# Performance work log

Measured on AMD Instinct MI355X. Metric: run time of the kernel, lower is better.

Reference implementation:

```python
import jax, jax.numpy as jnp
import numpy as np

N, B, T, H, M, DM, K = 256, 32, 128, 64, 8, 32, 3
IN_DIM = 1
OUT_DIM = 1
DEC_H = H + DM  # 96


def _p(key, shape):
    return jax.random.normal(key, shape, jnp.float32) / np.sqrt(shape[0]).astype(np.float32)


def setup_inputs() -> dict:
    key = jax.random.key(0)
    ks = jax.random.split(key, 10)
    gdi = 2 * K * (IN_DIM + H)      # 390
    ddi = 2 * K * (OUT_DIM + DEC_H)  # 582
    return {
        'x': jax.random.normal(ks[0], (B, T, N, IN_DIM), jnp.float32),
        'Memory': _p(ks[1], (M, DM)),
        'Wq': _p(ks[2], (H, DM)),
        'We1': _p(ks[3], (N, M)),
        'We2': _p(ks[4], (N, M)),
        'enc_gate_w': _p(ks[5], (gdi, 2 * H)), 'enc_gate_b': jnp.zeros((2 * H,), jnp.float32),
        'enc_upd_w': _p(ks[6], (gdi, H)), 'enc_upd_b': jnp.zeros((H,), jnp.float32),
        'dec_gate_w': _p(ks[7], (ddi, 2 * DEC_H)), 'dec_gate_b': jnp.zeros((2 * DEC_H,), jnp.float32),
        'dec_upd_w': _p(ks[8], (ddi, DEC_H)), 'dec_upd_b': jnp.zeros((DEC_H,), jnp.float32),
        'proj_w': _p(ks[9], (DEC_H, OUT_DIM)), 'proj_b': jnp.zeros((OUT_DIM,), jnp.float32),
    }


def _cheb(s):
    # Chebyshev polynomials T_0..T_{K-1} of support s: [I, s, 2 s T_{k-1} - T_{k-2}]
    polys = [jnp.eye(N, dtype=s.dtype), s]
    for _ in range(2, K):
        polys.append(2.0 * s @ polys[-1] - polys[-2])
    return polys


def _scaled_lap(e1, e2, gkey):
    # cosine-similarity graph -> straight-through gumbel hard selection -> scaled Laplacian
    norm = jnp.linalg.norm(e1, axis=1, keepdims=True) @ jnp.linalg.norm(e2, axis=1, keepdims=True).T
    g = (e1 @ e2.T) / (norm + 1e-6)
    g = (g + 1.0) / 2.0
    logits = jnp.stack([g, 1.0 - g], axis=-1)               # (N,N,2)
    y_soft = logits + jax.random.gumbel(gkey, logits.shape, logits.dtype)  # tau=1 (note: source skips softmax)
    y_hard = jax.nn.one_hot(jnp.argmax(y_soft, axis=-1), 2, dtype=logits.dtype)
    adj = (y_hard - jax.lax.stop_gradient(y_soft) + y_soft)[:, :, 0]
    eye = jnp.eye(N, dtype=adj.dtype)
    adj = adj * (1.0 - eye)                                  # zero diagonal
    d = jnp.sum(adj, axis=1)
    L = jnp.diag(d) - adj
    lam = L.max() - L.min()
    return 2.0 * L / lam - eye


def _gconv(x, S, w, b):
    # S: (2K,N,N) stacked cheb supports; x: (B,N,C)
    xg = jnp.einsum('knm,bmc->bnkc', S, x)
    xg = xg.reshape(xg.shape[0], xg.shape[1], -1)            # (B,N,2K*C), support-major like torch cat
    return xg @ w + b


def _cell(x, state, S, gw, gb, uw, ub, hid):
    zr = jax.nn.sigmoid(_gconv(jnp.concatenate([x, state], -1), S, gw, gb))
    z, r = zr[..., :hid], zr[..., hid:]
    hc = jnp.tanh(_gconv(jnp.concatenate([x, z * state], -1), S, uw, ub))
    return r * state + (1.0 - r) * hc


def reference(x, Memory, Wq, We1, We2, enc_gate_w, enc_gate_b, enc_upd_w, enc_upd_b,
              dec_gate_w, dec_gate_b, dec_upd_w, dec_upd_b, proj_w, proj_b):
    k1, k2 = jax.random.split(jax.random.key(42))
    e1, e2 = We1 @ Memory, We2 @ Memory
    S = jnp.stack(_cheb(_scaled_lap(e1, e2, k1)) + _cheb(_scaled_lap(e2, e1, k2)))  # (2K,N,N)

    # --- encoder (1 layer) over time ---
    def enc_step(state, xt):
        h = _cell(xt, state, S, enc_gate_w, enc_gate_b, enc_upd_w, enc_upd_b, H)
        return h, None
    h0 = jnp.zeros((x.shape[0], N, H), x.dtype)
    h_t, _ = jax.lax.scan(enc_step, h0, jnp.swapaxes(x, 0, 1))

    # --- memory attention query ---
    query = h_t @ Wq                                        # (B,N,DM)
    att = jax.nn.softmax(query @ Memory.T, axis=-1)         # (B,N,M)
    value = att @ Memory                                    # (B,N,DM)
    h_de = jnp.concatenate([h_t, value], -1)                # (B,N,DEC_H)

    go0 = jnp.zeros((x.shape[0], N, OUT_DIM), x.dtype)
    def dec_step(carry, _):
        state, go = carry
        h = _cell(go, state, S, dec_gate_w, dec_gate_b, dec_upd_w, dec_upd_b, DEC_H)
        go = h @ proj_w + proj_b
        return (h, go), go
    _, outs = jax.lax.scan(dec_step, (h_de, go0), None, length=T)
    return jnp.swapaxes(outs, 0, 1)                         # (B,T,N,OUT_DIM)
```

## Files before the change

kernel.cpp:

```cpp
#include <hip/hip_runtime.h>
#include <stdint.h>
#include <math.h>

#define NNODE 256
#define BATCH 32
#define TLEN  128
#define ROWS  8192

typedef unsigned short u16;
typedef short bf16x8 __attribute__((ext_vector_type(8)));
typedef float f32x4 __attribute__((ext_vector_type(4)));

__device__ inline u16 f2bf_rn(float v) {
  uint32_t u = __float_as_uint(v);
  u += 0x7fffu + ((u >> 16) & 1u);
  return (u16)(u >> 16);
}
__device__ inline float bf2f(u16 h) { return __uint_as_float(((uint32_t)h) << 16); }
__device__ inline void split2(float v, u16& hi, u16& lo) {
  hi = f2bf_rn(v);
  lo = f2bf_rn(v - bf2f(hi));
}

__device__ inline size_t pk_addr(int c, int b, int n) {
  return ((((size_t)(c >> 4) * 32 + b) * 8 + (n >> 5)) << 9) +
         (((size_t)((c & 15) | (((n >> 3) & 3) << 4))) << 3) + (n & 7);
}

__host__ __device__ inline uint32_t rotl32_(uint32_t v, int d) {
  return (v << d) | (v >> (32 - d));
}
__host__ __device__ inline void tf2x32(uint32_t k0, uint32_t k1, uint32_t x0,
                                       uint32_t x1, uint32_t* o0, uint32_t* o1) {
  uint32_t ks2 = k0 ^ k1 ^ 0x1BD11BDAu;
  x0 += k0; x1 += k1;
  x0 += x1; x1 = rotl32_(x1, 13); x1 ^= x0;
  x0 += x1; x1 = rotl32_(x1, 15); x1 ^= x0;
  x0 += x1; x1 = rotl32_(x1, 26); x1 ^= x0;
  x0 += x1; x1 = rotl32_(x1, 6);  x1 ^= x0;
  x0 += k1; x1 += ks2 + 1u;
  x0 += x1; x1 = rotl32_(x1, 17); x1 ^= x0;
  x0 += x1; x1 = rotl32_(x1, 29); x1 ^= x0;
  x0 += x1; x1 = rotl32_(x1, 16); x1 ^= x0;
  x0 += x1; x1 = rotl32_(x1, 24); x1 ^= x0;
  x0 += ks2; x1 += k0 + 2u;
  x0 += x1; x1 = rotl32_(x1, 13); x1 ^= x0;
  x0 += x1; x1 = rotl32_(x1, 15); x1 ^= x0;
  x0 += x1; x1 = rotl32_(x1, 26); x1 ^= x0;
  x0 += x1; x1 = rotl32_(x1, 6);  x1 ^= x0;
  x0 += k0; x1 += k1 + 3u;
  x0 += x1; x1 = rotl32_(x1, 17); x1 ^= x0;
  x0 += x1; x1 = rotl32_(x1, 29); x1 ^= x0;
  x0 += x1; x1 = rotl32_(x1, 16); x1 ^= x0;
  x0 += x1; x1 = rotl32_(x1, 24); x1 ^= x0;
  x0 += k1; x1 += ks2 + 4u;
  x0 += x1; x1 = rotl32_(x1, 13); x1 ^= x0;
  x0 += x1; x1 = rotl32_(x1, 15); x1 ^= x0;
  x0 += x1; x1 = rotl32_(x1, 26); x1 ^= x0;
  x0 += x1; x1 = rotl32_(x1, 6);  x1 ^= x0;
  x0 += ks2; x1 += k0 + 5u;
  *o0 = x0; *o1 = x1;
}

__device__ inline float gumbel_at(uint32_t k0, uint32_t k1, uint32_t idx) {
  uint32_t o0, o1;
  tf2x32(k0, k1, 0u, idx, &o0, &o1);
  uint32_t b = o0 ^ o1;
  float f = __uint_as_float((b >> 9) | 0x3f800000u) - 1.0f;
  const float tiny = 1.17549435e-38f;
  float u = fmaxf(tiny, f + tiny);
  return -logf(-logf(u));
}

__global__ __launch_bounds__(256) void setup_embed_kernel(
    const float* __restrict__ We1, const float* __restrict__ We2,
    const float* __restrict__ Mem, float* __restrict__ e1, float* __restrict__ e2,
    float* __restrict__ n1, float* __restrict__ n2) {
  int n = threadIdx.x;
  float a[8];
  float s;
  for (int m = 0; m < 8; ++m) a[m] = We1[n * 8 + m];
  s = 0.f;
  for (int j = 0; j < 32; ++j) {
    float v = 0.f;
    for (int m = 0; m < 8; ++m) v = fmaf(a[m], Mem[m * 32 + j], v);
    e1[n * 32 + j] = v;
    s = fmaf(v, v, s);
  }
  n1[n] = sqrtf(s);
  for (int m = 0; m < 8; ++m) a[m] = We2[n * 8 + m];
  s = 0.f;
  for (int j = 0; j < 32; ++j) {
    float v = 0.f;
    for (int m = 0; m < 8; ++m) v = fmaf(a[m], Mem[m * 32 + j], v);
    e2[n * 32 + j] = v;
    s = fmaf(v, v, s);
  }
  n2[n] = sqrtf(s);
}

__global__ void stats_init_kernel(int* stats) {
  stats[0] = 0;
  stats[1] = 0;
  stats[2] = 0x7fffffff;
}

__global__ __launch_bounds__(256) void adj_kernel(
    const float* __restrict__ eA, const float* __restrict__ eB,
    const float* __restrict__ nA, const float* __restrict__ nB,
    uint32_t k0, uint32_t k1, float* __restrict__ adj, float* __restrict__ deg,
    int* __restrict__ stats) {
  int i = blockIdx.x, j = threadIdx.x;
  float dot = 0.f;
  for (int c = 0; c < 32; ++c) dot = fmaf(eA[i * 32 + c], eB[j * 32 + c], dot);
  float g = dot / (nA[i] * nB[j] + 1e-6f);
  g = (g + 1.0f) * 0.5f;
  uint32_t f = ((uint32_t)(i * 256 + j)) * 2u;
  float g0 = gumbel_at(k0, k1, f);
  float g1 = gumbel_at(k0, k1, f + 1u);
  float a = ((g + g0) >= ((1.0f - g) + g1)) ? 1.0f : 0.0f;
  if (i == j) a = 0.0f;
  adj[i * 256 + j] = a;
  __shared__ float red[256];
  red[j] = a;
  __syncthreads();
  for (int s = 128; s > 0; s >>= 1) {
    if (j < s) red[j] += red[j + s];
    __syncthreads();
  }
  if (j == 0) {
    float d = red[0];
    deg[i] = d;
    atomicMax(&stats[0], (int)d);
    atomicMin(&stats[2], (int)d);
    if (d > 0.5f) atomicOr(&stats[1], 1);
  }
}

__global__ __launch_bounds__(256) void lap_kernel(const float* __restrict__ adj,
                                                  const float* __restrict__ deg,
                                                  const int* __restrict__ stats,
                                                  float* __restrict__ S1) {
  int i = blockIdx.x, j = threadIdx.x;
  float lmax = (float)stats[0];
  float lmin = stats[1] ? -1.0f : (float)stats[2];
  float lam = lmax - lmin;
  float L = (i == j) ? deg[i] : -adj[i * 256 + j];
  S1[i * 256 + j] = 2.0f * L / lam - ((i == j) ? 1.0f : 0.0f);
}

__global__ __launch_bounds__(256) void t2_kernel(const float* __restrict__ A,
                                                 float* __restrict__ Cout) {
  __shared__ __align__(16) float sAT[32][68];
  __shared__ __align__(16) float sB[32][68];
  int tid = threadIdx.x;
  int tc = tid & 15, tr = tid >> 4;
  int row0 = blockIdx.y * 64, col0 = blockIdx.x * 64;
  float acc[4][4] = {};
  for (int m0 = 0; m0 < 256; m0 += 32) {
    for (int i = tid; i < 2048; i += 256) {
      int r = i >> 5, c = i & 31;
      sAT[c][r] = A[(size_t)(row0 + r) * 256 + m0 + c];
    }
    for (int i = tid; i < 2048; i += 256) {
      int r = i >> 6, c = i & 63;
      sB[r][c] = A[(size_t)(m0 + r) * 256 + col0 + c];
    }
    __syncthreads();
#pragma unroll
    for (int kk = 0; kk < 32; ++kk) {
      float4 av = *(const float4*)&sAT[kk][tr * 4];
      float4 bv = *(const float4*)&sB[kk][tc * 4];
      float a[4] = {av.x, av.y, av.z, av.w};
      float b[4] = {bv.x, bv.y, bv.z, bv.w};
#pragma unroll
      for (int i = 0; i < 4; ++i)
#pragma unroll
        for (int j = 0; j < 4; ++j) acc[i][j] = fmaf(a[i], b[j], acc[i][j]);
    }
    __syncthreads();
  }
#pragma unroll
  for (int i = 0; i < 4; ++i) {
    int row = row0 + tr * 4 + i;
#pragma unroll
    for (int j = 0; j < 4; ++j) {
      int col = col0 + tc * 4 + j;
      Cout[(size_t)row * 256 + col] = 2.0f * acc[i][j] - ((row == col) ? 1.0f : 0.0f);
    }
  }
}

__global__ void cvt_s_packed(const float* __restrict__ S, u16* __restrict__ Sh,
                             u16* __restrict__ Sl) {
  int idx = blockIdx.x * 256 + threadIdx.x;
  if (idx >= 4 * 65536) return;
  int p = idx >> 16, rem = idx & 65535;
  int n = rem >> 8, m = rem & 255;
  int nt = n >> 4, li = n & 15;
  int mc = m >> 5, g = (m >> 3) & 3, j = m & 7;
  int lane = li | (g << 4);
  size_t a = (((size_t)(p * 16 + nt) * 8 + mc) << 9) + lane * 8 + j;
  u16 h, l;
  split2(S[idx], h, l);
  Sh[a] = h; Sl[a] = l;
}

__global__ void build_wfrag(const float* __restrict__ W, int C, int O, int hid,
                            u16* __restrict__ WfH, u16* __restrict__ WfL,
                            float* __restrict__ w0, float* __restrict__ wlast) {
  int idx = blockIdx.x * 256 + threadIdx.x;
  int nKC = hid / 32;
  if (idx < 5 * hid * O) {
    int kk = idx & 31;
    int rest = idx >> 5;
    int o = rest % O; rest /= O;
    int kc = rest % nKC;
    int p = rest / nKC;
    int korig = (p == 0) ? 0 : (p + (p >= 3 ? 1 : 0));
    int c = kc * 32 + kk;
    float v = 0.f;
    if (c > 0) {
      v = W[(size_t)(korig * C + c) * O + o];
      if (p == 0) v += W[(size_t)(3 * C + c) * O + o];
    }
    int ot = o >> 4, li = o & 15, g = kk >> 3, j = kk & 7;
    int lane = li | (g << 4);
    size_t a = (((size_t)(p * nKC + kc) * (O / 16) + ot) << 9) + lane * 8 + j;
    u16 h, l; split2(v, h, l);
    WfH[a] = h; WfL[a] = l;
  }
  if (idx < 5 * O) {
    int o = idx % O, p = idx / O;
    int korig = (p == 0) ? 0 : (p + (p >= 3 ? 1 : 0));
    float v0 = W[(size_t)(korig * C + 0) * O + o];
    if (p == 0) v0 += W[(size_t)(3 * C + 0) * O + o];
    w0[p * O + o] = v0;
    float vl = W[(size_t)(korig * C + hid) * O + o];
    if (p == 0) vl += W[(size_t)(3 * C + hid) * O + o];
    wlast[p * O + o] = vl;
  }
}

__global__ void zero_kernel(uint4* __restrict__ p, int n4) {
  for (int i = blockIdx.x * blockDim.x + threadIdx.x; i < n4;
       i += gridDim.x * blockDim.x)
    p[i] = make_uint4(0, 0, 0, 0);
}

__global__ void enc_init(const float* __restrict__ x, float* __restrict__ hf,
                         u16* __restrict__ pkh, u16* __restrict__ pkl) {
  int idx = blockIdx.x * 256 + threadIdx.x;
  if (idx >= 65 * ROWS) return;
  int c = idx / ROWS, col = idx % ROWS;
  int b = col >> 8, n = col & 255;
  float v = (c == 0) ? x[(size_t)b * (TLEN * NNODE) + n] : 0.f;
  hf[idx] = v;
  if (c == 0) {
    u16 h, l; split2(v, h, l);
    size_t a = pk_addr(0, b, n);
    pkh[a] = h; pkl[a] = l;
  }
}

__global__ __launch_bounds__(128) void attn2(const float* __restrict__ hEf,
                                             const float* __restrict__ Wq,
                                             const float* __restrict__ Mem,
                                             float* __restrict__ hDf,
                                             u16* __restrict__ pkh,
                                             u16* __restrict__ pkl) {
  int col = blockIdx.x * 128 + threadIdx.x;
  int b = col >> 8, n = col & 255;
  float h[64];
  for (int c = 0; c < 64; ++c) h[c] = hEf[(size_t)(1 + c) * ROWS + col];
  float q[32];
  for (int j = 0; j < 32; ++j) {
    float s = 0.f;
    for (int c = 0; c < 64; ++c) s = fmaf(h[c], Wq[c * 32 + j], s);
    q[j] = s;
  }
  float l[8], mx = -3.402823466e38f;
  for (int m = 0; m < 8; ++m) {
    float s = 0.f;
    for (int j = 0; j < 32; ++j) s = fmaf(q[j], Mem[m * 32 + j], s);
    l[m] = s;
    mx = fmaxf(mx, s);
  }
  float se = 0.f;
  for (int m = 0; m < 8; ++m) { l[m] = expf(l[m] - mx); se += l[m]; }
  float val[32];
  for (int j = 0; j < 32; ++j) {
    float v = 0.f;
    for (int m = 0; m < 8; ++m) v = fmaf(l[m] / se, Mem[m * 32 + j], v);
    val[j] = v;
  }
  for (int c = 0; c < 97; ++c) {
    float v = (c == 0) ? 0.f : ((c <= 64) ? h[c - 1] : val[c - 65]);
    hDf[(size_t)c * ROWS + col] = v;
    u16 hh, ll; split2(v, hh, ll);
    size_t a = pk_addr(c, b, n);
    pkh[a] = hh; pkl[a] = ll;
  }
}

template <int C, int HID, int CPAD, int O, int NKC, int MT1, int MODE>
__global__ __launch_bounds__(1024, 4) void fused_step(
    const float* __restrict__ AF,
    const u16* __restrict__ ApkH, const u16* __restrict__ ApkL,
    const u16* __restrict__ SpkH, const u16* __restrict__ SpkL,
    const u16* __restrict__ WpkH, const u16* __restrict__ WpkL,
    const float* __restrict__ w0, const float* __restrict__ wlast,
    const float* __restrict__ bias,
    float* __restrict__ HF, float* __restrict__ outF,
    u16* __restrict__ outPkH, u16* __restrict__ outPkL,
    float* __restrict__ rbuf,
    const float* __restrict__ xsrc, int tnext,
    const float* __restrict__ pw, const float* __restrict__ pb,
    float* __restrict__ outp, int tcur) {
  constexpr int MT2 = O / 16;
  constexpr int MT1A = (MT1 + 1) / 2;
  constexpr int CH0SLOT = HID + 1;

  __shared__ __align__(16) u16 Gh[2][5][16][CPAD];
  __shared__ __align__(16) u16 Gl[2][5][16][CPAD];
  __shared__ float projL[(MODE == 2) ? 2 : 1][16][(MODE == 2) ? 100 : 1];

  const int tid = threadIdx.x;
  const int wid = tid >> 6, lane = tid & 63;
  const int g = lane >> 4, li = lane & 15;
  const int cg = wid >> 3, pp = wid & 3, half = (wid >> 2) & 1;
  const int bid0 = (int)blockIdx.x;
  const int bidx = ((bid0 & 7) << 5) | (bid0 >> 3);
  const int col0 = bidx * 32;
  const int b = col0 >> 8;
  const int n0 = (col0 & 255) + cg * 16;
  const int nt = n0 >> 4;

  for (int i = tid; i < 32 * C; i += 1024) {
    int c = i >> 5, q = i & 31;
    float v = AF[(size_t)c * ROWS + col0 + q];
    u16 h, l; split2(v, h, l);
    int slot = (c == 0) ? CH0SLOT : c;
    Gh[q >> 4][0][q & 15][slot] = h;
    Gl[q >> 4][0][q & 15][slot] = l;
  }
  if (tid < 32) {
    Gh[tid >> 4][0][tid & 15][0] = 0;
    Gl[tid >> 4][0][tid & 15][0] = 0;
  }

  f32x4 acc1[MT1A];
#pragma unroll
  for (int i = 0; i < MT1A; ++i) acc1[i] = (f32x4){0.f, 0.f, 0.f, 0.f};

#pragma unroll 2
  for (int mc = 0; mc < 8; ++mc) {
    size_t sa = (((size_t)(pp * 16 + nt) * 8 + mc) << 9) + lane * 8;
    bf16x8 sbh = *(const bf16x8*)(SpkH + sa);
    bf16x8 sbl = *(const bf16x8*)(SpkL + sa);
#pragma unroll
    for (int i = 0; i < MT1A; ++i) {
      const int mt = half * MT1A + i;
      if (mt < MT1) {
        size_t aa = (((size_t)(mt * 32 + b) * 8 + mc) << 9) + lane * 8;
        bf16x8 ah = *(const bf16x8*)(ApkH + aa);
        bf16x8 al = *(const bf16x8*)(ApkL + aa);
        acc1[i] = __builtin_amdgcn_mfma_f32_16x16x32_bf16(ah, sbh, acc1[i], 0, 0, 0);
        acc1[i] = __builtin_amdgcn_mfma_f32_16x16x32_bf16(ah, sbl, acc1[i], 0, 0, 0);
        acc1[i] = __builtin_amdgcn_mfma_f32_16x16x32_bf16(al, sbh, acc1[i], 0, 0, 0);
      }
    }
  }

  {
    const int p = pp + 1;
#pragma unroll
    for (int i = 0; i < MT1A; ++i) {
      const int mt = half * MT1A + i;
      if (mt < MT1) {
        int cq = mt * 16 + 4 * g;
        u16 h4[4], l4[4];
#pragma unroll
        for (int r = 0; r < 4; ++r) split2(acc1[i][r], h4[r], l4[r]);
        if (cq == 0) {
          Gh[cg][p][li][CH0SLOT] = h4[0];
          Gl[cg][p][li][CH0SLOT] = l4[0];
          h4[0] = 0; l4[0] = 0;
        }
        if (cq + 3 <= HID) {
          uint2 vh, vl;
          vh.x = (uint32_t)h4[0] | ((uint32_t)h4[1] << 16);
          vh.y = (uint32_t)h4[2] | ((uint32_t)h4[3] << 16);
          vl.x = (uint32_t)l4[0] | ((uint32_t)l4[1] << 16);
          vl.y = (uint32_t)l4[2] | ((uint32_t)l4[3] << 16);
          *(uint2*)&Gh[cg][p][li][cq] = vh;
          *(uint2*)&Gl[cg][p][li][cq] = vl;
        } else {
#pragma unroll
          for (int r = 0; r < 4; ++r) {
            int c = cq + r;
            if (c >= 1 && c <= HID) {
              Gh[cg][p][li][c] = h4[r];
              Gl[cg][p][li][c] = l4[r];
            }
          }
        }
      }
    }
  }
  __syncthreads();

  const int mt2 = wid;
  f32x4 acc2[2];
  acc2[0] = (f32x4){0.f, 0.f, 0.f, 0.f};
  acc2[1] = (f32x4){0.f, 0.f, 0.f, 0.f};
  if (mt2 < MT2) {
#pragma unroll
    for (int p = 0; p < 5; ++p) {
#pragma unroll
      for (int kc = 0; kc < NKC; ++kc) {
        bf16x8 bh[2], bl[2];
#pragma unroll
        for (int c2 = 0; c2 < 2; ++c2) {
          bh[c2] = *(const bf16x8*)&Gh[c2][p][li][kc * 32 + g * 8];
          bl[c2] = *(const bf16x8*)&Gl[c2][p][li][kc * 32 + g * 8];
        }
        size_t wa = (((size_t)(p * NKC + kc) * MT2 + mt2) << 9) + lane * 8;
        bf16x8 wh = *(const bf16x8*)(WpkH + wa);
        bf16x8 wl = *(const bf16x8*)(WpkL + wa);
#pragma unroll
        for (int c2 = 0; c2 < 2; ++c2) {
          acc2[c2] = __builtin_amdgcn_mfma_f32_16x16x32_bf16(wh, bh[c2], acc2[c2], 0, 0, 0);
          acc2[c2] = __builtin_amdgcn_mfma_f32_16x16x32_bf16(wh, bl[c2], acc2[c2], 0, 0, 0);
          acc2[c2] = __builtin_amdgcn_mfma_f32_16x16x32_bf16(wl, bh[c2], acc2[c2], 0, 0, 0);
        }
      }
    }
  }

  float ch0v[2][5], clv[2][5];
#pragma unroll
  for (int c2 = 0; c2 < 2; ++c2)
#pragma unroll
    for (int p = 0; p < 5; ++p) {
      ch0v[c2][p] = (p == 0)
          ? AF[col0 + c2 * 16 + li]
          : (bf2f(Gh[c2][p][li][CH0SLOT]) + bf2f(Gl[c2][p][li][CH0SLOT]));
      clv[c2][p] = bf2f(Gh[c2][p][li][HID]) + bf2f(Gl[c2][p][li][HID]);
    }

  if (mt2 < MT2) {
#pragma unroll
    for (int c2 = 0; c2 < 2; ++c2) {
      const int colx = col0 + c2 * 16 + li;
      const int ncolx = colx & 255;
#pragma unroll
      for (int r = 0; r < 4; ++r) {
        int o = mt2 * 16 + 4 * g + r;
        float v = acc2[c2][r] + bias[o];
#pragma unroll
        for (int p = 0; p < 5; ++p) {
          v = fmaf(w0[p * O + o], ch0v[c2][p], v);
          v = fmaf(wlast[p * O + o], clv[c2][p], v);
        }
        if (MODE == 0) {
          float s = 1.0f / (1.0f + expf(-v));
          if (o < HID) {
            float u = s * HF[(size_t)(1 + o) * ROWS + colx];
            outF[(size_t)(1 + o) * ROWS + colx] = u;
            u16 h_, l_; split2(u, h_, l_);
            size_t a = pk_addr(1 + o, b, ncolx);
            outPkH[a] = h_; outPkL[a] = l_;
          } else {
            rbuf[(size_t)(o - HID) * ROWS + colx] = s;
          }
        } else {
          float hc = tanhf(v);
          float hp = HF[(size_t)(1 + o) * ROWS + colx];
          float rr = rbuf[(size_t)o * ROWS + colx];
          float hn = rr * hp + (1.0f - rr) * hc;
          HF[(size_t)(1 + o) * ROWS + colx] = hn;
          u16 h_, l_; split2(hn, h_, l_);
          size_t a = pk_addr(1 + o, b, ncolx);
          outPkH[a] = h_; outPkL[a] = l_;
          if (MODE == 2) projL[c2][li][o] = hn;
        }
      }
    }
  }

  if (MODE == 0) {
    if (tid < 32) {
      int cc = col0 + tid;
      float x0 = AF[cc];
      outF[cc] = x0;
      u16 h_, l_; split2(x0, h_, l_);
      size_t a = pk_addr(0, b, cc & 255);
      outPkH[a] = h_; outPkL[a] = l_;
    }
  }
  if (MODE == 1) {
    __syncthreads();
    if (tid < 32) {
      int cc = col0 + tid;
      int n = cc & 255;
      float xv = (tnext >= 0)
          ? xsrc[(size_t)b * (TLEN * NNODE) + (size_t)tnext * NNODE + n]
          : HF[cc];
      HF[cc] = xv;
      u16 h_, l_; split2(xv, h_, l_);
      size_t a = pk_addr(0, b, n);
      outPkH[a] = h_; outPkL[a] = l_;
    }
  }
  if (MODE == 2) {
    __syncthreads();
    if (tid < 32) {
      int cc = col0 + tid;
      int n = cc & 255;
      float s = pb[0];
#pragma unroll
      for (int o = 0; o < HID; ++o) s = fmaf(pw[o], projL[tid >> 4][tid & 15][o], s);
      HF[cc] = s;
      u16 h_, l_; split2(s, h_, l_);
      size_t a = pk_addr(0, b, n);
      outPkH[a] = h_; outPkL[a] = l_;
      outp[((size_t)b * TLEN + tcur) * NNODE + n] = s;
    }
  }
}

extern "C" void kernel_launch(void* const* d_in, const int* in_sizes, int n_in,
                              void* d_out, int out_size, void* d_ws, size_t ws_size,
                              hipStream_t stream) {
  (void)in_sizes; (void)n_in; (void)out_size; (void)ws_size;
  const float* x   = (const float*)d_in[0];
  const float* Mem = (const float*)d_in[1];
  const float* Wq  = (const float*)d_in[2];
  const float* We1 = (const float*)d_in[3];
  const float* We2 = (const float*)d_in[4];
  const float* egw = (const float*)d_in[5];
  const float* egb = (const float*)d_in[6];
  const float* euw = (const float*)d_in[7];
  const float* eub = (const float*)d_in[8];
  const float* dgw = (const float*)d_in[9];
  const float* dgb = (const float*)d_in[10];
  const float* duw = (const float*)d_in[11];
  const float* dub = (const float*)d_in[12];
  const float* pw  = (const float*)d_in[13];
  const float* pb  = (const float*)d_in[14];
  float* out = (float*)d_out;

  float* ws = (float*)d_ws;
  size_t off = 0;
  auto allocf = [&](size_t nf) {
    float* p = ws + off;
    off += (nf + 63) & ~(size_t)63;
    return p;
  };
  auto allocu = [&](size_t nu) { return (u16*)allocf((nu + 1) / 2); };

  float* Sf  = allocf(4 * 65536);
  float* e1  = allocf(8192);
  float* e2  = allocf(8192);
  float* n1  = allocf(256);
  float* n2  = allocf(256);
  float* adj = allocf(65536);
  float* deg = allocf(256);
  int* stats = (int*)allocf(64);
  float* rb  = allocf((size_t)96 * ROWS);
  float* hEf = allocf((size_t)65 * ROWS);
  float* uEf = allocf((size_t)65 * ROWS);
  float* hDf = allocf((size_t)97 * ROWS);
  float* uDf = allocf((size_t)97 * ROWS);
  float* w0gE = allocf(5 * 128);
  float* w0uE = allocf(5 * 64);
  float* w0gD = allocf(5 * 192);
  float* w0uD = allocf(5 * 96);
  float* wlgE = allocf(5 * 128);
  float* wluE = allocf(5 * 64);
  float* wlgD = allocf(5 * 192);
  float* wluD = allocf(5 * 96);

  u16* SpkH = allocu((size_t)4 * 65536);
  u16* SpkL = allocu((size_t)4 * 65536);
  u16* WgEh = allocu((size_t)5 * 2 * 8 * 512);
  u16* WgEl = allocu((size_t)5 * 2 * 8 * 512);
  u16* WuEh = allocu((size_t)5 * 2 * 4 * 512);
  u16* WuEl = allocu((size_t)5 * 2 * 4 * 512);
  u16* WgDh = allocu((size_t)5 * 3 * 12 * 512);
  u16* WgDl = allocu((size_t)5 * 3 * 12 * 512);
  u16* WuDh = allocu((size_t)5 * 3 * 6 * 512);
  u16* WuDl = allocu((size_t)5 * 3 * 6 * 512);

  const size_t PKE = (size_t)5 * 32 * 8 * 512;
  const size_t PKD = (size_t)7 * 32 * 8 * 512;
  u16* hEpkH = allocu(PKE);
  u16* hEpkL = allocu(PKE);
  u16* uEpkH = allocu(PKE);
  u16* uEpkL = allocu(PKE);
  u16* hDpkH = allocu(PKD);
  u16* hDpkL = allocu(PKD);
  u16* uDpkH = allocu(PKD);
  u16* uDpkL = allocu(PKD);
  const size_t PKTOT = 4 * PKE + 4 * PKD;

  uint32_t ka0, ka1, kb0, kb1;
  tf2x32(0u, 42u, 0u, 0u, &ka0, &ka1);
  tf2x32(0u, 42u, 0u, 1u, &kb0, &kb1);

  zero_kernel<<<1024, 256, 0, stream>>>((uint4*)hEpkH, (int)(PKTOT / 8));
  setup_embed_kernel<<<1, 256, 0, stream>>>(We1, We2, Mem, e1, e2, n1, n2);
  stats_init_kernel<<<1, 1, 0, stream>>>(stats);
  adj_kernel<<<256, 256, 0, stream>>>(e1, e2, n1, n2, ka0, ka1, adj, deg, stats);
  lap_kernel<<<256, 256, 0, stream>>>(adj, deg, stats, Sf);
  t2_kernel<<<dim3(4, 4), 256, 0, stream>>>(Sf, Sf + 65536);
  stats_init_kernel<<<1, 1, 0, stream>>>(stats);
  adj_kernel<<<256, 256, 0, stream>>>(e2, e1, n2, n1, kb0, kb1, adj, deg, stats);
  lap_kernel<<<256, 256, 0, stream>>>(adj, deg, stats, Sf + 2 * 65536);
  t2_kernel<<<dim3(4, 4), 256, 0, stream>>>(Sf + 2 * 65536, Sf + 3 * 65536);
  cvt_s_packed<<<1024, 256, 0, stream>>>(Sf, SpkH, SpkL);
  build_wfrag<<<(5 * 64 * 128 + 255) / 256, 256, 0, stream>>>(egw, 65, 128, 64, WgEh, WgEl, w0gE, wlgE);
  build_wfrag<<<(5 * 64 * 64 + 255) / 256, 256, 0, stream>>>(euw, 65, 64, 64, WuEh, WuEl, w0uE, wluE);
  build_wfrag<<<(5 * 96 * 192 + 255) / 256, 256, 0, stream>>>(dgw, 97, 192, 96, WgDh, WgDl, w0gD, wlgD);
  build_wfrag<<<(5 * 96 * 96 + 255) / 256, 256, 0, stream>>>(duw, 97, 96, 96, WuDh, WuDl, w0uD, wluD);

  enc_init<<<(65 * ROWS + 255) / 256, 256, 0, stream>>>(x, hEf, hEpkH, hEpkL);
  for (int t = 0; t < TLEN; ++t) {
    fused_step<65, 64, 72, 128, 2, 5, 0><<<256, 1024, 0, stream>>>(
        hEf, hEpkH, hEpkL, SpkH, SpkL, WgEh, WgEl, w0gE, wlgE, egb,
        hEf, uEf, uEpkH, uEpkL, rb, nullptr, -1, nullptr, nullptr, nullptr, 0);
    fused_step<65, 64, 72, 64, 2, 5, 1><<<256, 1024, 0, stream>>>(
        uEf, uEpkH, uEpkL, SpkH, SpkL, WuEh, WuEl, w0uE, wluE, eub,
        hEf, hEf, hEpkH, hEpkL, rb,
        x, (t + 1 < TLEN) ? (t + 1) : -1, nullptr, nullptr, nullptr, 0);
  }

  attn2<<<64, 128, 0, stream>>>(hEf, Wq, Mem, hDf, hDpkH, hDpkL);

  for (int t = 0; t < TLEN; ++t) {
    fused_step<97, 96, 104, 192, 3, 7, 0><<<256, 1024, 0, stream>>>(
        hDf, hDpkH, hDpkL, SpkH, SpkL, WgDh, WgDl, w0gD, wlgD, dgb,
        hDf, uDf, uDpkH, uDpkL, rb, nullptr, -1, nullptr, nullptr, nullptr, 0);
    fused_step<97, 96, 104, 96, 3, 7, 2><<<256, 1024, 0, stream>>>(
        uDf, uDpkH, uDpkL, SpkH, SpkL, WuDh, WuDl, w0uD, wluD, dub,
        hDf, hDf, hDpkH, hDpkL, rb,
        nullptr, -1, pw, pb, out, t);
  }
}
```

Baseline: 8.907 ms.

## Drop fp32 state copies and keep recurrent state only in split-bf16 packed form

Removes the fp32 channel-major state buffers (hEf/uEf/hDf/uDf). Every stage now reads the previous hidden state and gate inputs by reconstructing hi+lo bf16 pairs from the packed buffers, so each step writes and reads less global memory and no longer re-splits fp32 data. The shared-memory G tiles move from padded [16][CPAD] rows to a blocked 8-element layout, which changes LDS bank access for the 16-byte fragment reads. The price is a small precision loss, since state passes through a two-term bf16 representation instead of full fp32. The packed-address reads in the prologue are also more scattered than the old contiguous fp32 rows.

```diff
diff --git a/kernel.cpp b/kernel.cpp
--- a/kernel.cpp
+++ b/kernel.cpp
@@ -248,31 +248,30 @@
     p[i] = make_uint4(0, 0, 0, 0);
 }
 
-__global__ void enc_init(const float* __restrict__ x, float* __restrict__ hf,
+__global__ void enc_init(const float* __restrict__ x,
                          u16* __restrict__ pkh, u16* __restrict__ pkl) {
-  int idx = blockIdx.x * 256 + threadIdx.x;
-  if (idx >= 65 * ROWS) return;
-  int c = idx / ROWS, col = idx % ROWS;
+  int col = blockIdx.x * 256 + threadIdx.x;
+  if (col >= ROWS) return;
   int b = col >> 8, n = col & 255;
-  float v = (c == 0) ? x[(size_t)b * (TLEN * NNODE) + n] : 0.f;
-  hf[idx] = v;
-  if (c == 0) {
-    u16 h, l; split2(v, h, l);
-    size_t a = pk_addr(0, b, n);
-    pkh[a] = h; pkl[a] = l;
-  }
-}
-
-__global__ __launch_bounds__(128) void attn2(const float* __restrict__ hEf,
+  float v = x[(size_t)b * (TLEN * NNODE) + n];
+  u16 h, l; split2(v, h, l);
+  size_t a = pk_addr(0, b, n);
+  pkh[a] = h; pkl[a] = l;
+}
+
+__global__ __launch_bounds__(128) void attn2(const u16* __restrict__ hEh,
+                                             const u16* __restrict__ hEl,
                                              const float* __restrict__ Wq,
                                              const float* __restrict__ Mem,
-                                             float* __restrict__ hDf,
                                              u16* __restrict__ pkh,
                                              u16* __restrict__ pkl) {
   int col = blockIdx.x * 128 + threadIdx.x;
   int b = col >> 8, n = col & 255;
   float h[64];
-  for (int c = 0; c < 64; ++c) h[c] = hEf[(size_t)(1 + c) * ROWS + col];
+  for (int c = 0; c < 64; ++c) {
+    size_t a = pk_addr(1 + c, b, n);
+    h[c] = bf2f(hEh[a]) + bf2f(hEl[a]);
+  }
   float q[32];
   for (int j = 0; j < 32; ++j) {
     float s = 0.f;
@@ -296,22 +295,20 @@
   }
   for (int c = 0; c < 97; ++c) {
     float v = (c == 0) ? 0.f : ((c <= 64) ? h[c - 1] : val[c - 65]);
-    hDf[(size_t)c * ROWS + col] = v;
     u16 hh, ll; split2(v, hh, ll);
     size_t a = pk_addr(c, b, n);
     pkh[a] = hh; pkl[a] = ll;
   }
 }
 
-template <int C, int HID, int CPAD, int O, int NKC, int MT1, int MODE>
+template <int C, int HID, int O, int NKC, int MT1, int MODE>
 __global__ __launch_bounds__(1024, 4) void fused_step(
-    const float* __restrict__ AF,
     const u16* __restrict__ ApkH, const u16* __restrict__ ApkL,
     const u16* __restrict__ SpkH, const u16* __restrict__ SpkL,
     const u16* __restrict__ WpkH, const u16* __restrict__ WpkL,
     const float* __restrict__ w0, const float* __restrict__ wlast,
     const float* __restrict__ bias,
-    float* __restrict__ HF, float* __restrict__ outF,
+    const u16* __restrict__ stH, const u16* __restrict__ stL,
     u16* __restrict__ outPkH, u16* __restrict__ outPkL,
     float* __restrict__ rbuf,
     const float* __restrict__ xsrc, int tnext,
@@ -320,33 +317,39 @@
   constexpr int MT2 = O / 16;
   constexpr int MT1A = (MT1 + 1) / 2;
   constexpr int CH0SLOT = HID + 1;
-
-  __shared__ __align__(16) u16 Gh[2][5][16][CPAD];
-  __shared__ __align__(16) u16 Gl[2][5][16][CPAD];
-  __shared__ float projL[(MODE == 2) ? 2 : 1][16][(MODE == 2) ? 100 : 1];
+  constexpr int KS8 = (HID + 9) / 8;
+
+  __shared__ __align__(16) u16 GhR[(size_t)2 * 5 * KS8 * 16 * 8];
+  __shared__ __align__(16) u16 GlR[(size_t)2 * 5 * KS8 * 16 * 8];
+  __shared__ float projL[(MODE == 2) ? 32 * 100 : 4];
+
+  auto Gidx = [](int c2, int p, int li, int slot) -> size_t {
+    return (((size_t)((c2 * 5 + p) * KS8 + (slot >> 3)) * 16 + li) << 3) +
+           (slot & 7);
+  };
 
   const int tid = threadIdx.x;
   const int wid = tid >> 6, lane = tid & 63;
   const int g = lane >> 4, li = lane & 15;
-  const int cg = wid >> 3, pp = wid & 3, half = (wid >> 2) & 1;
+  const int cgi = wid >> 3, pp = wid & 3, half = (wid >> 2) & 1;
   const int bid0 = (int)blockIdx.x;
   const int bidx = ((bid0 & 7) << 5) | (bid0 >> 3);
   const int col0 = bidx * 32;
   const int b = col0 >> 8;
-  const int n0 = (col0 & 255) + cg * 16;
+  const int nb = col0 & 255;
+  const int n0 = nb + cgi * 16;
   const int nt = n0 >> 4;
 
   for (int i = tid; i < 32 * C; i += 1024) {
     int c = i >> 5, q = i & 31;
-    float v = AF[(size_t)c * ROWS + col0 + q];
-    u16 h, l; split2(v, h, l);
+    size_t a = pk_addr(c, b, nb + q);
     int slot = (c == 0) ? CH0SLOT : c;
-    Gh[q >> 4][0][q & 15][slot] = h;
-    Gl[q >> 4][0][q & 15][slot] = l;
+    GhR[Gidx(q >> 4, 0, q & 15, slot)] = ApkH[a];
+    GlR[Gidx(q >> 4, 0, q & 15, slot)] = ApkL[a];
   }
   if (tid < 32) {
-    Gh[tid >> 4][0][tid & 15][0] = 0;
-    Gl[tid >> 4][0][tid & 15][0] = 0;
+    GhR[Gidx(tid >> 4, 0, tid & 15, 0)] = 0;
+    GlR[Gidx(tid >> 4, 0, tid & 15, 0)] = 0;
   }
 
   f32x4 acc1[MT1A];
@@ -383,8 +386,8 @@
 #pragma unroll
         for (int r = 0; r < 4; ++r) split2(acc1[i][r], h4[r], l4[r]);
         if (cq == 0) {
-          Gh[cg][p][li][CH0SLOT] = h4[0];
-          Gl[cg][p][li][CH0SLOT] = l4[0];
+          GhR[Gidx(cgi, p, li, CH0SLOT)] = h4[0];
+          GlR[Gidx(cgi, p, li, CH0SLOT)] = l4[0];
           h4[0] = 0; l4[0] = 0;
         }
         if (cq + 3 <= HID) {
@@ -393,15 +396,15 @@
           vh.y = (uint32_t)h4[2] | ((uint32_t)h4[3] << 16);
           vl.x = (uint32_t)l4[0] | ((uint32_t)l4[1] << 16);
           vl.y = (uint32_t)l4[2] | ((uint32_t)l4[3] << 16);
-          *(uint2*)&Gh[cg][p][li][cq] = vh;
-          *(uint2*)&Gl[cg][p][li][cq] = vl;
+          *(uint2*)&GhR[Gidx(cgi, p, li, cq)] = vh;
+          *(uint2*)&GlR[Gidx(cgi, p, li, cq)] = vl;
         } else {
 #pragma unroll
           for (int r = 0; r < 4; ++r) {
             int c = cq + r;
             if (c >= 1 && c <= HID) {
-              Gh[cg][p][li][c] = h4[r];
-              Gl[cg][p][li][c] = l4[r];
+              GhR[Gidx(cgi, p, li, c)] = h4[r];
+              GlR[Gidx(cgi, p, li, c)] = l4[r];
             }
           }
         }
@@ -422,8 +425,8 @@
         bf16x8 bh[2], bl[2];
 #pragma unroll
         for (int c2 = 0; c2 < 2; ++c2) {
-          bh[c2] = *(const bf16x8*)&Gh[c2][p][li][kc * 32 + g * 8];
-          bl[c2] = *(const bf16x8*)&Gl[c2][p][li][kc * 32 + g * 8];
+          bh[c2] = *(const bf16x8*)&GhR[Gidx(c2, p, li, kc * 32 + g * 8)];
+          bl[c2] = *(const bf16x8*)&GlR[Gidx(c2, p, li, kc * 32 + g * 8)];
         }
         size_t wa = (((size_t)(p * NKC + kc) * MT2 + mt2) << 9) + lane * 8;
         bf16x8 wh = *(const bf16x8*)(WpkH + wa);
@@ -443,17 +446,21 @@
   for (int c2 = 0; c2 < 2; ++c2)
 #pragma unroll
     for (int p = 0; p < 5; ++p) {
-      ch0v[c2][p] = (p == 0)
-          ? AF[col0 + c2 * 16 + li]
-          : (bf2f(Gh[c2][p][li][CH0SLOT]) + bf2f(Gl[c2][p][li][CH0SLOT]));
-      clv[c2][p] = bf2f(Gh[c2][p][li][HID]) + bf2f(Gl[c2][p][li][HID]);
+      if (p == 0) {
+        size_t a = pk_addr(0, b, nb + c2 * 16 + li);
+        ch0v[c2][p] = bf2f(ApkH[a]) + bf2f(ApkL[a]);
+      } else {
+        ch0v[c2][p] = bf2f(GhR[Gidx(c2, p, li, CH0SLOT)]) +
+                      bf2f(GlR[Gidx(c2, p, li, CH0SLOT)]);
+      }
+      clv[c2][p] = bf2f(GhR[Gidx(c2, p, li, HID)]) + bf2f(GlR[Gidx(c2, p, li, HID)]);
     }
 
   if (mt2 < MT2) {
 #pragma unroll
     for (int c2 = 0; c2 < 2; ++c2) {
+      const int ncolx = nb + c2 * 16 + li;
       const int colx = col0 + c2 * 16 + li;
-      const int ncolx = colx & 255;
 #pragma unroll
       for (int r = 0; r < 4; ++r) {
         int o = mt2 * 16 + 4 * g + r;
@@ -463,27 +470,25 @@
           v = fmaf(w0[p * O + o], ch0v[c2][p], v);
           v = fmaf(wlast[p * O + o], clv[c2][p], v);
         }
+        size_t a = pk_addr(1 + o, b, ncolx);
         if (MODE == 0) {
           float s = 1.0f / (1.0f + expf(-v));
           if (o < HID) {
-            float u = s * HF[(size_t)(1 + o) * ROWS + colx];
-            outF[(size_t)(1 + o) * ROWS + colx] = u;
+            float hrec = bf2f(stH[a]) + bf2f(stL[a]);
+            float u = s * hrec;
             u16 h_, l_; split2(u, h_, l_);
-            size_t a = pk_addr(1 + o, b, ncolx);
             outPkH[a] = h_; outPkL[a] = l_;
           } else {
             rbuf[(size_t)(o - HID) * ROWS + colx] = s;
           }
         } else {
           float hc = tanhf(v);
-          float hp = HF[(size_t)(1 + o) * ROWS + colx];
+          float hp = bf2f(stH[a]) + bf2f(stL[a]);
           float rr = rbuf[(size_t)o * ROWS + colx];
           float hn = rr * hp + (1.0f - rr) * hc;
-          HF[(size_t)(1 + o) * ROWS + colx] = hn;
           u16 h_, l_; split2(hn, h_, l_);
-          size_t a = pk_addr(1 + o, b, ncolx);
           outPkH[a] = h_; outPkL[a] = l_;
-          if (MODE == 2) projL[c2][li][o] = hn;
+          if (MODE == 2) projL[((size_t)c2 * 16 + li) * 100 + o] = hn;
         }
       }
     }
@@ -491,23 +496,15 @@
 
   if (MODE == 0) {
     if (tid < 32) {
-      int cc = col0 + tid;
-      float x0 = AF[cc];
-      outF[cc] = x0;
-      u16 h_, l_; split2(x0, h_, l_);
-      size_t a = pk_addr(0, b, cc & 255);
-      outPkH[a] = h_; outPkL[a] = l_;
+      size_t a = pk_addr(0, b, nb + tid);
+      outPkH[a] = ApkH[a];
+      outPkL[a] = ApkL[a];
     }
   }
   if (MODE == 1) {
-    __syncthreads();
-    if (tid < 32) {
-      int cc = col0 + tid;
-      int n = cc & 255;
-      float xv = (tnext >= 0)
-          ? xsrc[(size_t)b * (TLEN * NNODE) + (size_t)tnext * NNODE + n]
-          : HF[cc];
-      HF[cc] = xv;
+    if (tnext >= 0 && tid < 32) {
+      int n = nb + tid;
+      float xv = xsrc[(size_t)b * (TLEN * NNODE) + (size_t)tnext * NNODE + n];
       u16 h_, l_; split2(xv, h_, l_);
       size_t a = pk_addr(0, b, n);
       outPkH[a] = h_; outPkL[a] = l_;
@@ -516,12 +513,10 @@
   if (MODE == 2) {
     __syncthreads();
     if (tid < 32) {
-      int cc = col0 + tid;
-      int n = cc & 255;
+      int n = nb + tid;
       float s = pb[0];
 #pragma unroll
-      for (int o = 0; o < HID; ++o) s = fmaf(pw[o], projL[tid >> 4][tid & 15][o], s);
-      HF[cc] = s;
+      for (int o = 0; o < HID; ++o) s = fmaf(pw[o], projL[(size_t)tid * 100 + o], s);
       u16 h_, l_; split2(s, h_, l_);
       size_t a = pk_addr(0, b, n);
       outPkH[a] = h_; outPkL[a] = l_;
@@ -569,10 +564,6 @@
   float* deg = allocf(256);
   int* stats = (int*)allocf(64);
   float* rb  = allocf((size_t)96 * ROWS);
-  float* hEf = allocf((size_t)65 * ROWS);
-  float* uEf = allocf((size_t)65 * ROWS);
-  float* hDf = allocf((size_t)97 * ROWS);
-  float* uDf = allocf((size_t)97 * ROWS);
   float* w0gE = allocf(5 * 128);
   float* w0uE = allocf(5 * 64);
   float* w0gD = allocf(5 * 192);
@@ -625,26 +616,26 @@
   build_wfrag<<<(5 * 96 * 192 + 255) / 256, 256, 0, stream>>>(dgw, 97, 192, 96, WgDh, WgDl, w0gD, wlgD);
   build_wfrag<<<(5 * 96 * 96 + 255) / 256, 256, 0, stream>>>(duw, 97, 96, 96, WuDh, WuDl, w0uD, wluD);
 
-  enc_init<<<(65 * ROWS + 255) / 256, 256, 0, stream>>>(x, hEf, hEpkH, hEpkL);
+  enc_init<<<32, 256, 0, stream>>>(x, hEpkH, hEpkL);
   for (int t = 0; t < TLEN; ++t) {
-    fused_step<65, 64, 72, 128, 2, 5, 0><<<256, 1024, 0, stream>>>(
-        hEf, hEpkH, hEpkL, SpkH, SpkL, WgEh, WgEl, w0gE, wlgE, egb,
-        hEf, uEf, uEpkH, uEpkL, rb, nullptr, -1, nullptr, nullptr, nullptr, 0);
-    fused_step<65, 64, 72, 64, 2, 5, 1><<<256, 1024, 0, stream>>>(
-        uEf, uEpkH, uEpkL, SpkH, SpkL, WuEh, WuEl, w0uE, wluE, eub,
-        hEf, hEf, hEpkH, hEpkL, rb,
+    fused_step<65, 64, 128, 2, 5, 0><<<256, 1024, 0, stream>>>(
+        hEpkH, hEpkL, SpkH, SpkL, WgEh, WgEl, w0gE, wlgE, egb,
+        hEpkH, hEpkL, uEpkH, uEpkL, rb, nullptr, -1, nullptr, nullptr, nullptr, 0);
+    fused_step<65, 64, 64, 2, 5, 1><<<256, 1024, 0, stream>>>(
+        uEpkH, uEpkL, SpkH, SpkL, WuEh, WuEl, w0uE, wluE, eub,
+        hEpkH, hEpkL, hEpkH, hEpkL, rb,
         x, (t + 1 < TLEN) ? (t + 1) : -1, nullptr, nullptr, nullptr, 0);
   }
 
-  attn2<<<64, 128, 0, stream>>>(hEf, Wq, Mem, hDf, hDpkH, hDpkL);
+  attn2<<<64, 128, 0, stream>>>(hEpkH, hEpkL, Wq, Mem, hDpkH, hDpkL);
 
   for (int t = 0; t < TLEN; ++t) {
-    fused_step<97, 96, 104, 192, 3, 7, 0><<<256, 1024, 0, stream>>>(
-        hDf, hDpkH, hDpkL, SpkH, SpkL, WgDh, WgDl, w0gD, wlgD, dgb,
-        hDf, uDf, uDpkH, uDpkL, rb, nullptr, -1, nullptr, nullptr, nullptr, 0);
-    fused_step<97, 96, 104, 96, 3, 7, 2><<<256, 1024, 0, stream>>>(
-        uDf, uDpkH, uDpkL, SpkH, SpkL, WuDh, WuDl, w0uD, wluD, dub,
-        hDf, hDf, hDpkH, hDpkL, rb,
+    fused_step<97, 96, 192, 3, 7, 0><<<256, 1024, 0, stream>>>(
+        hDpkH, hDpkL, SpkH, SpkL, WgDh, WgDl, w0gD, wlgD, dgb,
+        hDpkH, hDpkL, uDpkH, uDpkL, rb, nullptr, -1, nullptr, nullptr, nullptr, 0);
+    fused_step<97, 96, 96, 3, 7, 2><<<256, 1024, 0, stream>>>(
+        uDpkH, uDpkL, SpkH, SpkL, WuDh, WuDl, w0uD, wluD, dub,
+        hDpkH, hDpkL, hDpkH, hDpkL, rb,
         nullptr, -1, pw, pb, out, t);
   }
 }
```

Result: faster. 8.008 ms, median of 2 (-10.1%).
